# Optimization experiments

Hardware: AMD Instinct MI355X
Metric: run time of the kernel (lower is better)

## Reference

```python
import jax, jax.numpy as jnp
import numpy as np
import math

D_MODEL = 1024
N_HEADS = 16
SEQ = 2048
BATCH = 2


def setup_inputs() -> dict:
    key = jax.random.key(0)
    ks = jax.random.split(key, 7)
    scale = 1.0 / math.sqrt(D_MODEL)
    return {
        "q": jax.random.normal(ks[0], (SEQ, BATCH, D_MODEL), jnp.float32),
        "k": jax.random.normal(ks[1], (SEQ, BATCH, D_MODEL), jnp.float32),
        "v": jax.random.normal(ks[2], (SEQ, BATCH, D_MODEL), jnp.float32),
        "in_proj_w": jax.random.normal(ks[3], (3 * D_MODEL, D_MODEL), jnp.float32) * scale,
        "in_proj_b": jax.random.normal(ks[4], (3 * D_MODEL,), jnp.float32) * 0.01,
        "out_proj_w": jax.random.normal(ks[5], (D_MODEL, D_MODEL), jnp.float32) * scale,
        "out_proj_b": jax.random.normal(ks[6], (D_MODEL,), jnp.float32) * 0.01,
    }


def reference(q, k, v, in_proj_w, in_proj_b, out_proj_w, out_proj_b):
    # q, k, v: (S, B, D) seq-first layout as in the torch module
    S, B, D = q.shape
    H = N_HEADS
    dk = D // H
    wq, wk, wv = jnp.split(in_proj_w, 3, axis=0)   # each (D, D)
    bq, bk, bv = jnp.split(in_proj_b, 3, axis=0)   # each (D,)
    qp = q @ wq.T + bq
    kp = k @ wk.T + bk
    vp = v @ wv.T + bv
    # (S, B, D) -> (S, B*H, dk) -> (B*H, S, dk)
    def to_heads(x, s):
        return x.reshape(s, B * H, dk).transpose(1, 0, 2)
    qh = to_heads(qp, S)
    kh = to_heads(kp, k.shape[0])
    vh = to_heads(vp, v.shape[0])
    # scores: (B*H, Sq, Sk)
    scores = jnp.einsum('bqd,bkd->bqk', qh, kh) / math.sqrt(dk)
    probs = jax.nn.softmax(scores, axis=-1)
    attn = jnp.einsum('bqk,bkd->bqd', probs, vh)   # (B*H, S, dk)
    # (B*H, S, dk) -> (S, B*H, dk) -> (S*B, D)
    attn = attn.transpose(1, 0, 2).reshape(S * B, D)
    out = attn @ out_proj_w.T + out_proj_b
    return out.reshape(S, B, D)
```

## Files before the change

### kernel.cpp

```cpp
#include <hip/hip_runtime.h>
#include <math.h>

#define SEQ    2048
#define BATCH  2
#define DMODEL 1024
#define NHEADS 16
#define DK     64

typedef __attribute__((ext_vector_type(8))) short  bf16x8;
typedef __attribute__((ext_vector_type(4))) float  f32x4;
typedef __attribute__((ext_vector_type(8))) unsigned short u16x8;

#define GLD16(gp, lp) __builtin_amdgcn_global_load_lds(                      \
    (__attribute__((address_space(1))) void*)(gp),                            \
    (__attribute__((address_space(3))) void*)(lp), 16, 0, 0)

__device__ inline unsigned short f2bf(float f) {
    unsigned int u = __float_as_uint(f);
    u += 0x7fffu + ((u >> 16) & 1u);
    return (unsigned short)(u >> 16);
}

__device__ inline unsigned int pk2bf(float a, float b) {
#if __has_builtin(__builtin_amdgcn_cvt_pk_bf16_f32)
    typedef __attribute__((ext_vector_type(2))) __bf16 v2bf;
    v2bf r = __builtin_amdgcn_cvt_pk_bf16_f32(a, b);
    unsigned int u; __builtin_memcpy(&u, &r, 4); return u;
#else
    return (unsigned int)f2bf(a) | ((unsigned int)f2bf(b) << 16);
#endif
}

__device__ inline float fast_exp2(float x) {
#if __has_builtin(__builtin_amdgcn_exp2f)
    return __builtin_amdgcn_exp2f(x);
#else
    return __expf(x * 0.69314718055994531f);
#endif
}

#define WS_QB   0u
#define WS_KB   4194304u
#define WS_VB   8388608u
#define WS_WIB  12582912u
#define WS_WOB  15728640u
#define WS_QH   16777216u
#define WS_KH   20971520u
#define WS_VT   25165824u
#define WS_ATT  29360128u

__global__ __launch_bounds__(256) void cast_w_kernel(
    const float* __restrict__ w_in, const float* __restrict__ w_out,
    unsigned short* __restrict__ ws)
{
    const int gid = blockIdx.x * 256 + threadIdx.x;
    const float* src; unsigned short* dst;
    if (gid < 393216) { int g = gid;          src = w_in  + (size_t)g*8; dst = ws + WS_WIB + (size_t)g*8; }
    else              { int g = gid - 393216; src = w_out + (size_t)g*8; dst = ws + WS_WOB + (size_t)g*8; }
    float4 a = *(const float4*)src;
    float4 b = *(const float4*)(src + 4);
    u16x8 o;
    o[0]=f2bf(a.x); o[1]=f2bf(a.y); o[2]=f2bf(a.z); o[3]=f2bf(a.w);
    o[4]=f2bf(b.x); o[5]=f2bf(b.y); o[6]=f2bf(b.z); o[7]=f2bf(b.w);
    *(u16x8*)dst = o;
}

__global__ __launch_bounds__(256) void qkv_gemm_kernel(
    const float* __restrict__ qp, const float* __restrict__ kp,
    const float* __restrict__ vp, const unsigned short* __restrict__ ws_in,
    const float* __restrict__ bias, unsigned short* __restrict__ ws_out)
{
    __shared__ unsigned short As[128*32];
    __shared__ unsigned short Bs[128*32];

    const int t    = threadIdx.x;
    const int lane = t & 63;
    const int w    = t >> 6;
    const int lrow = lane & 15;
    const int quad = lane >> 4;
    const int wm   = (w >> 1) * 64;
    const int wn   = (w & 1) * 64;

    const int bid = blockIdx.x;
    const int xcd = bid & 7;
    const int idx = bid >> 3;
    const int xg  = xcd * 3 + idx % 3;
    const int yg  = idx / 3;

    const int n0    = xg * 128;
    const int m0    = yg * 128;
    const int which = n0 >> 10;

    const float* Af = (which == 0) ? qp : (which == 1) ? kp : vp;
    const unsigned short* B = ws_in + WS_WIB;

    const int srow = t >> 2;
    const int scc  = (t & 3) ^ ((t >> 3) & 3);
    const float* pA0 = Af + (size_t)(m0 + srow) * 1024 + scc * 8;
    const float* pA1 = Af + (size_t)(m0 + 64 + srow) * 1024 + scc * 8;
    const unsigned short* gB0 = B + (size_t)(n0 + srow) * 1024 + scc * 8;
    const unsigned short* gB1 = B + (size_t)(n0 + 64 + srow) * 1024 + scc * 8;

    f32x4 acc[4][4] = {};

    float4 a0 = *(const float4*)pA0;
    float4 a1 = *(const float4*)(pA0 + 4);
    float4 c0 = *(const float4*)pA1;
    float4 c1 = *(const float4*)(pA1 + 4);
    pA0 += 32; pA1 += 32;

    #pragma unroll 1
    for (int kt = 0; kt < 1024; kt += 32) {
        __syncthreads();
        GLD16(gB0, Bs + (size_t)t * 8);
        GLD16(gB1, Bs + (size_t)(t + 256) * 8);
        {
            uint4 pa, pc;
            pa.x = pk2bf(a0.x, a0.y); pa.y = pk2bf(a0.z, a0.w);
            pa.z = pk2bf(a1.x, a1.y); pa.w = pk2bf(a1.z, a1.w);
            pc.x = pk2bf(c0.x, c0.y); pc.y = pk2bf(c0.z, c0.w);
            pc.z = pk2bf(c1.x, c1.y); pc.w = pk2bf(c1.z, c1.w);
            *(uint4*)(As + (size_t)t * 8)         = pa;
            *(uint4*)(As + (size_t)(t + 256) * 8) = pc;
        }
        gB0 += 32; gB1 += 32;
        __syncthreads();

        if (kt + 32 < 1024) {
            a0 = *(const float4*)pA0;
            a1 = *(const float4*)(pA0 + 4);
            c0 = *(const float4*)pA1;
            c1 = *(const float4*)(pA1 + 4);
            pA0 += 32; pA1 += 32;
        }

        bf16x8 af[4], bf[4];
        #pragma unroll
        for (int mt = 0; mt < 4; ++mt) {
            const int r = wm + mt*16 + lrow;
            af[mt] = *(const bf16x8*)(As + r*32 + ((quad ^ ((r>>1)&3))*8));
        }
        #pragma unroll
        for (int nt = 0; nt < 4; ++nt) {
            const int r = wn + nt*16 + lrow;
            bf[nt] = *(const bf16x8*)(Bs + r*32 + ((quad ^ ((r>>1)&3))*8));
        }
        #pragma unroll
        for (int mt = 0; mt < 4; ++mt)
            #pragma unroll
            for (int nt = 0; nt < 4; ++nt)
                acc[mt][nt] = __builtin_amdgcn_mfma_f32_16x16x32_bf16(
                    af[mt], bf[nt], acc[mt][nt], 0, 0, 0);
    }

    unsigned short* dstQK = ws_out + WS_QH + (size_t)which * 4194304u;
    unsigned short* dstV  = ws_out + WS_VT;
    const float qscale = 0.18033688011112042f;

    #pragma unroll
    for (int nt = 0; nt < 4; ++nt) {
        const int n = n0 + wn + nt*16 + lrow;
        const float bn = bias[n];
        const int h = (n & 1023) >> 6;
        const int d = n & 63;
        #pragma unroll
        for (int mt = 0; mt < 4; ++mt) {
            if (which < 2) {
                #pragma unroll
                for (int r = 0; r < 4; ++r) {
                    const int m = m0 + wm + mt*16 + quad*4 + r;
                    const int s = m >> 1, b = m & 1;
                    float val = acc[mt][nt][r] + bn;
                    if (which == 0) val *= qscale;
                    dstQK[((size_t)((b<<4) + h) * 2048 + s) * 64 + d] = f2bf(val);
                }
            } else {
                const int m_base = m0 + wm + mt*16 + quad*4;
                const int s0 = m_base >> 1;
                unsigned int pk0 = pk2bf(acc[mt][nt][0] + bn, acc[mt][nt][2] + bn);
                unsigned int pk1 = pk2bf(acc[mt][nt][1] + bn, acc[mt][nt][3] + bn);
                *(unsigned int*)(dstV + ((size_t)h*64 + d)*2048 + s0)        = pk0;
                *(unsigned int*)(dstV + ((size_t)(16 + h)*64 + d)*2048 + s0) = pk1;
            }
        }
    }
}

__global__ __launch_bounds__(256) void attn_mfma_kernel(
    const unsigned short* __restrict__ qh, const unsigned short* __restrict__ kh,
    const unsigned short* __restrict__ vt, unsigned short* __restrict__ attn)
{
    __shared__ unsigned short Ks[2][64*64];
    __shared__ unsigned short Vts[2][64*64];
    __shared__ unsigned short Ps[64*64];

    const int t    = threadIdx.x;
    const int lane = t & 63;
    const int w    = t >> 6;
    const int lrow = lane & 15;
    const int quad = lane >> 4;

    const int bid = blockIdx.x;
    const int swz = (bid & 7) * 128 + (bid >> 3);
    const int qt  = swz & 31;
    const int bh  = swz >> 5;

    const unsigned short* Qg = qh + ((size_t)bh * 2048 + qt * 64) * 64;
    const unsigned short* Kb = kh + (size_t)bh * 2048 * 64;
    const unsigned short* Vb = vt + (size_t)bh * 64 * 2048;

    #pragma unroll
    for (int i = 0; i < 2; ++i) {
        const int c = i*256 + t;
        const int row = c >> 3, cc = (c & 7) ^ (row & 7);
        GLD16(Qg + (size_t)row*64   + cc*8, &Ks[1][0]  + (size_t)c*8);
        GLD16(Kb + (size_t)row*64   + cc*8, &Ks[0][0]  + (size_t)c*8);
        GLD16(Vb + (size_t)row*2048 + cc*8, &Vts[0][0] + (size_t)c*8);
    }
    __syncthreads();

    bf16x8 qf[2];
    #pragma unroll
    for (int kk = 0; kk < 2; ++kk) {
        const int r = w*16 + lrow;
        qf[kk] = *(const bf16x8*)(&Ks[1][0] + r*64 + (((kk*4+quad) ^ (r&7))*8));
    }
    __syncthreads();

    f32x4 O[4] = {};
    float l_i = 0.f;

    int buf = 0;
    #pragma unroll 1
    for (int ktile = 0; ktile < 32; ++ktile) {
        if (ktile < 31) {
            const unsigned short* Kg = Kb + (size_t)(ktile + 1) * 64 * 64;
            const unsigned short* Vg = Vb + (size_t)(ktile + 1) * 64;
            unsigned short* Kn = &Ks[buf ^ 1][0];
            unsigned short* Vn = &Vts[buf ^ 1][0];
            #pragma unroll
            for (int i = 0; i < 2; ++i) {
                const int c = i*256 + t;
                const int row = c >> 3, cc = (c & 7) ^ (row & 7);
                GLD16(Kg + (size_t)row*64   + cc*8, Kn + (size_t)c*8);
                GLD16(Vg + (size_t)row*2048 + cc*8, Vn + (size_t)c*8);
            }
        }
        const unsigned short* Kc = &Ks[buf][0];
        const unsigned short* Vc = &Vts[buf][0];

        bf16x8 kf[4][2], vf[2][4];
        #pragma unroll
        for (int m = 0; m < 4; ++m) {
            const int r = m*16 + lrow;
            kf[m][0] = *(const bf16x8*)(Kc + r*64 + (((  quad) ^ (r&7))*8));
            kf[m][1] = *(const bf16x8*)(Kc + r*64 + (((4+quad) ^ (r&7))*8));
        }
        #pragma unroll
        for (int dt = 0; dt < 4; ++dt) {
            const int r = dt*16 + lrow;
            vf[0][dt] = *(const bf16x8*)(Vc + r*64 + (((  quad) ^ (r&7))*8));
            vf[1][dt] = *(const bf16x8*)(Vc + r*64 + (((4+quad) ^ (r&7))*8));
        }

        const int prow = w*16 + lrow;
        __builtin_amdgcn_s_setprio(1);
        #pragma unroll
        for (int m = 0; m < 4; ++m) {
            f32x4 s = {};
            s = __builtin_amdgcn_mfma_f32_16x16x32_bf16(kf[m][0], qf[0], s, 0, 0, 0);
            s = __builtin_amdgcn_mfma_f32_16x16x32_bf16(kf[m][1], qf[1], s, 0, 0, 0);
            const float p0 = fast_exp2(s[0]);
            const float p1 = fast_exp2(s[1]);
            const float p2 = fast_exp2(s[2]);
            const float p3 = fast_exp2(s[3]);
            l_i += (p0 + p1) + (p2 + p3);
            uint2 pk;
            pk.x = pk2bf(p0, p1);
            pk.y = pk2bf(p2, p3);
            const int sc = (m*2 + (quad >> 1)) ^ (prow & 7);
            *(uint2*)(Ps + prow*64 + sc*8 + (quad & 1)*4) = pk;
        }
        __builtin_amdgcn_s_setprio(0);

        #pragma unroll
        for (int kk = 0; kk < 2; ++kk) {
            bf16x8 pf;
            {
                const int r = w*16 + lrow;
                pf = *(const bf16x8*)(Ps + r*64 + (((kk*4+quad) ^ (r&7))*8));
            }
            __builtin_amdgcn_s_setprio(1);
            #pragma unroll
            for (int dt = 0; dt < 4; ++dt)
                O[dt] = __builtin_amdgcn_mfma_f32_16x16x32_bf16(
                    vf[kk][dt], pf, O[dt], 0, 0, 0);
            __builtin_amdgcn_s_setprio(0);
        }

        __syncthreads();
        buf ^= 1;
    }

    l_i += __shfl_xor(l_i, 16, 64);
    l_i += __shfl_xor(l_i, 32, 64);

    const int b_ = bh >> 4, h_ = bh & 15;
    const float inv = 1.f / l_i;
    const int s_ = qt*64 + w*16 + lrow;
    unsigned short* dst = attn + ((size_t)(s_*2 + b_)) * 1024 + h_*64;
    #pragma unroll
    for (int dt = 0; dt < 4; ++dt) {
        uint2 pk;
        pk.x = pk2bf(O[dt][0]*inv, O[dt][1]*inv);
        pk.y = pk2bf(O[dt][2]*inv, O[dt][3]*inv);
        *(uint2*)(dst + dt*16 + quad*4) = pk;
    }
}

__global__ __launch_bounds__(256) void out_gemm_kernel(
    const unsigned short* __restrict__ A, const unsigned short* __restrict__ B,
    const float* __restrict__ bias, float* __restrict__ out)
{
    __shared__ unsigned short As[64*32];
    __shared__ unsigned short Bs[128*32];

    const int t    = threadIdx.x;
    const int lane = t & 63;
    const int w    = t >> 6;
    const int lrow = lane & 15;
    const int quad = lane >> 4;
    const int wn   = (w >> 1) * 64;
    const int wm   = (w & 1) * 32;

    const int bid = blockIdx.x;
    const int n0  = (bid & 7) * 128;
    const int m0  = (bid >> 3) * 64;

    const int srow = t >> 2;
    const int scc  = (t & 3) ^ ((t >> 3) & 3);
    const unsigned short* gA0 = A + (size_t)(m0 + srow) * 1024 + scc * 8;
    const unsigned short* gB0 = B + (size_t)(n0 + srow) * 1024 + scc * 8;
    const unsigned short* gB1 = B + (size_t)(n0 + 64 + srow) * 1024 + scc * 8;

    f32x4 acc[2][4] = {};

    #pragma unroll 1
    for (int kt = 0; kt < 1024; kt += 32) {
        __syncthreads();
        GLD16(gA0, As + (size_t)t * 8);
        GLD16(gB0, Bs + (size_t)t * 8);
        GLD16(gB1, Bs + (size_t)(t + 256) * 8);
        gA0 += 32; gB0 += 32; gB1 += 32;
        __syncthreads();

        bf16x8 af[2], bf[4];
        #pragma unroll
        for (int mt = 0; mt < 2; ++mt) {
            const int r = wm + mt*16 + lrow;
            af[mt] = *(const bf16x8*)(As + r*32 + ((quad ^ ((r>>1)&3))*8));
        }
        #pragma unroll
        for (int nt = 0; nt < 4; ++nt) {
            const int r = wn + nt*16 + lrow;
            bf[nt] = *(const bf16x8*)(Bs + r*32 + ((quad ^ ((r>>1)&3))*8));
        }
        #pragma unroll
        for (int mt = 0; mt < 2; ++mt)
            #pragma unroll
            for (int nt = 0; nt < 4; ++nt)
                acc[mt][nt] = __builtin_amdgcn_mfma_f32_16x16x32_bf16(
                    af[mt], bf[nt], acc[mt][nt], 0, 0, 0);
    }

    #pragma unroll
    for (int nt = 0; nt < 4; ++nt) {
        const int n = n0 + wn + nt*16 + lrow;
        const float bn = bias[n];
        #pragma unroll
        for (int mt = 0; mt < 2; ++mt) {
            #pragma unroll
            for (int r = 0; r < 4; ++r) {
                const int m = m0 + wm + mt*16 + quad*4 + r;
                out[(size_t)m * 1024 + n] = acc[mt][nt][r] + bn;
            }
        }
    }
}

extern "C" void kernel_launch(void* const* d_in, const int* in_sizes, int n_in,
                              void* d_out, int out_size, void* d_ws, size_t ws_size,
                              hipStream_t stream) {
    const float* q     = (const float*)d_in[0];
    const float* k     = (const float*)d_in[1];
    const float* v     = (const float*)d_in[2];
    const float* w_in  = (const float*)d_in[3];
    const float* b_in  = (const float*)d_in[4];
    const float* w_out = (const float*)d_in[5];
    const float* b_out = (const float*)d_in[6];
    float* out = (float*)d_out;

    unsigned short* ws = (unsigned short*)d_ws;

    cast_w_kernel<<<2048, 256, 0, stream>>>(w_in, w_out, ws);
    qkv_gemm_kernel<<<768, 256, 0, stream>>>(q, k, v, ws, b_in, ws);
    attn_mfma_kernel<<<1024, 256, 0, stream>>>(
        ws + WS_QH, ws + WS_KH, ws + WS_VT, ws + WS_ATT);
    out_gemm_kernel<<<512, 256, 0, stream>>>(
        ws + WS_ATT, ws + WS_WOB, b_out, out);
}
```

Measured before the change: 228.5 us.

## Split QK^T across waves by key slice, sharing P through LDS

Each wave now computes scores for its own 16-key slice against all 64 queries, instead of all 64 keys against its own 16 queries. It keeps all Q fragments in registers and loads only two K fragments per tile, so per-wave K LDS reads drop fourfold. The P tile written to shared memory is now produced by different waves, which requires an extra block barrier per key tile before the PV MFMAs. Row sums are combined across waves through LDS at the end. This trades fewer LDS reads for an added barrier per iteration and more VGPRs for the Q fragments.

```diff
diff --git a/kernel.cpp b/kernel.cpp
--- a/kernel.cpp
+++ b/kernel.cpp
@@ -219,16 +219,20 @@
     }
     __syncthreads();
 
-    bf16x8 qf[2];
-    #pragma unroll
-    for (int kk = 0; kk < 2; ++kk) {
-        const int r = w*16 + lrow;
-        qf[kk] = *(const bf16x8*)(&Ks[1][0] + r*64 + (((kk*4+quad) ^ (r&7))*8));
+    bf16x8 qf[4][2];
+    #pragma unroll
+    for (int n = 0; n < 4; ++n) {
+        const int r = n*16 + lrow;
+        #pragma unroll
+        for (int kk = 0; kk < 2; ++kk)
+            qf[n][kk] = *(const bf16x8*)(&Ks[1][0] + r*64 + (((kk*4+quad) ^ (r&7))*8));
     }
     __syncthreads();
 
     f32x4 O[4] = {};
-    float l_i = 0.f;
+    float l4[4] = {0.f, 0.f, 0.f, 0.f};
+
+    const int rk = w*16 + lrow;
 
     int buf = 0;
     #pragma unroll 1
@@ -249,13 +253,9 @@
         const unsigned short* Kc = &Ks[buf][0];
         const unsigned short* Vc = &Vts[buf][0];
 
-        bf16x8 kf[4][2], vf[2][4];
-        #pragma unroll
-        for (int m = 0; m < 4; ++m) {
-            const int r = m*16 + lrow;
-            kf[m][0] = *(const bf16x8*)(Kc + r*64 + (((  quad) ^ (r&7))*8));
-            kf[m][1] = *(const bf16x8*)(Kc + r*64 + (((4+quad) ^ (r&7))*8));
-        }
+        bf16x8 kf0 = *(const bf16x8*)(Kc + rk*64 + (((  quad) ^ (rk&7))*8));
+        bf16x8 kf1 = *(const bf16x8*)(Kc + rk*64 + (((4+quad) ^ (rk&7))*8));
+        bf16x8 vf[2][4];
         #pragma unroll
         for (int dt = 0; dt < 4; ++dt) {
             const int r = dt*16 + lrow;
@@ -263,25 +263,30 @@
             vf[1][dt] = *(const bf16x8*)(Vc + r*64 + (((4+quad) ^ (r&7))*8));
         }
 
-        const int prow = w*16 + lrow;
         __builtin_amdgcn_s_setprio(1);
         #pragma unroll
-        for (int m = 0; m < 4; ++m) {
+        for (int n = 0; n < 4; ++n) {
             f32x4 s = {};
-            s = __builtin_amdgcn_mfma_f32_16x16x32_bf16(kf[m][0], qf[0], s, 0, 0, 0);
-            s = __builtin_amdgcn_mfma_f32_16x16x32_bf16(kf[m][1], qf[1], s, 0, 0, 0);
+            s = __builtin_amdgcn_mfma_f32_16x16x32_bf16(kf0, qf[n][0], s, 0, 0, 0);
+            s = __builtin_amdgcn_mfma_f32_16x16x32_bf16(kf1, qf[n][1], s, 0, 0, 0);
             const float p0 = fast_exp2(s[0]);
             const float p1 = fast_exp2(s[1]);
             const float p2 = fast_exp2(s[2]);
             const float p3 = fast_exp2(s[3]);
-            l_i += (p0 + p1) + (p2 + p3);
+            l4[n] += (p0 + p1) + (p2 + p3);
             uint2 pk;
             pk.x = pk2bf(p0, p1);
             pk.y = pk2bf(p2, p3);
-            const int sc = (m*2 + (quad >> 1)) ^ (prow & 7);
+            const int prow = n*16 + lrow;
+            const int sc = (w*2 + (quad >> 1)) ^ (prow & 7);
             *(uint2*)(Ps + prow*64 + sc*8 + (quad & 1)*4) = pk;
         }
         __builtin_amdgcn_s_setprio(0);
+
+        __builtin_amdgcn_sched_barrier(0);
+        asm volatile("s_waitcnt lgkmcnt(0)" ::: "memory");
+        __builtin_amdgcn_s_barrier();
+        __builtin_amdgcn_sched_barrier(0);
 
         #pragma unroll
         for (int kk = 0; kk < 2; ++kk) {
@@ -302,11 +307,23 @@
         buf ^= 1;
     }
 
-    l_i += __shfl_xor(l_i, 16, 64);
-    l_i += __shfl_xor(l_i, 32, 64);
+    #pragma unroll
+    for (int n = 0; n < 4; ++n) {
+        l4[n] += __shfl_xor(l4[n], 16, 64);
+        l4[n] += __shfl_xor(l4[n], 32, 64);
+    }
+    float* Lsc = (float*)Ps;
+    if (quad == 0) {
+        #pragma unroll
+        for (int n = 0; n < 4; ++n)
+            Lsc[w*64 + n*16 + lrow] = l4[n];
+    }
+    __syncthreads();
+    const int myq = w*16 + lrow;
+    const float l = Lsc[myq] + Lsc[64 + myq] + Lsc[128 + myq] + Lsc[192 + myq];
 
     const int b_ = bh >> 4, h_ = bh & 15;
-    const float inv = 1.f / l_i;
+    const float inv = 1.f / l;
     const int s_ = qt*64 + w*16 + lrow;
     unsigned short* dst = attn + ((size_t)(s_*2 + b_)) * 1024 + h_*64;
     #pragma unroll
```

Result: slower. 240.1 us (+5.1%).
